# Kernel optimization log

Hardware: AMD Instinct MI355X
Metric: run time of the kernel (lower is better)

## Reference

```python
import jax, jax.numpy as jnp
import numpy as np

B, C_IN, H, W = 128, 2, 64, 64
K = 50  # value-iteration steps


def _conv(x, w, b=None):
    # NCHW input, OIHW weights, stride 1, SAME padding (odd kernel)
    y = jax.lax.conv_general_dilated(
        x, w, window_strides=(1, 1), padding='SAME',
        dimension_numbers=('NCHW', 'OIHW', 'NCHW'))
    if b is not None:
        y = y + b[None, :, None, None]
    return y


def setup_inputs() -> dict:
    key = jax.random.key(0)
    ks = jax.random.split(key, 10)
    pos_x = jax.random.randint(ks[0], (B,), 0, H, dtype=jnp.int32)
    pos_y = jax.random.randint(ks[1], (B,), 0, W, dtype=jnp.int32)
    # channel 0 encodes agent position (single >0 entry); channel 1 is the obstacle/goal map
    ch0 = jnp.zeros((B, H, W), jnp.float32).at[jnp.arange(B), pos_x, pos_y].set(1.0)
    ch1 = jax.random.normal(ks[2], (B, H, W), jnp.float32)
    x = jnp.stack([ch0, ch1], axis=1)  # [B, 2, H, W]
    sc = lambda *s: 1.0 / np.sqrt(np.prod(s[1:])) if len(s) > 1 else 0.1
    h_w = jax.random.normal(ks[3], (150, C_IN, 3, 3), jnp.float32) * sc(150, C_IN, 3, 3)
    h_b = jax.random.normal(ks[4], (150,), jnp.float32) * 0.1
    r_w = jax.random.normal(ks[5], (1, 150, 3, 3), jnp.float32) * sc(1, 150, 3, 3)
    r_b = jax.random.normal(ks[6], (1,), jnp.float32) * 0.1
    q_w = jax.random.normal(ks[7], (10, 2, 3, 3), jnp.float32) * sc(10, 2, 3, 3)
    q_b = jax.random.normal(ks[8], (10,), jnp.float32) * 0.1
    fc_w = jax.random.normal(ks[9], (8, 10), jnp.float32) * sc(8, 10)
    return {'x': x, 'pos_x': pos_x, 'pos_y': pos_y,
            'h_w': h_w, 'h_b': h_b, 'r_w': r_w, 'r_b': r_b,
            'q_w': q_w, 'q_b': q_b, 'fc_w': fc_w}


def reference(x, pos_x, pos_y, h_w, h_b, r_w, r_b, q_w, q_b, fc_w):
    h = _conv(x, h_w, h_b)            # [B, 150, H, W]
    r = _conv(h, r_w, r_b)            # [B, 1, H, W]
    v0 = jnp.zeros_like(r)

    def vi_step(v, _):
        q = _conv(jnp.concatenate([r, v], axis=1), q_w, q_b)  # [B, 10, H, W]
        return jnp.max(q, axis=1, keepdims=True), None

    v, _ = jax.lax.scan(vi_step, v0, None, length=K)
    q = _conv(jnp.concatenate([r, v], axis=1), q_w, q_b)      # [B, 10, H, W]
    q_at = q[jnp.arange(q.shape[0]), :, pos_x, pos_y]         # [B, 10]
    return q_at @ fc_w.T                                       # [B, 8]
```

## Files before the change

kernel.cpp:

```cpp
#include <hip/hip_runtime.h>

#define KI 50

#define X1_OFF 4624
#define R_OFF 9248
#define W_OFF 13736
#define LDS_TOT 14178

__device__ __forceinline__ void vi_step(const float* __restrict__ cur, float* __restrict__ nxt,
                                        int row, int c0,
                                        const float (&qr)[10][8], const float (&qwv)[10][9]) {
    float nb[3][12];
#pragma unroll
    for (int dy = 0; dy < 3; ++dy) {
        const float* lp = cur + (row + dy) * 68 + c0;
        float4 a0 = *(const float4*)lp;
        float4 a1 = *(const float4*)(lp + 4);
        float4 a2 = *(const float4*)(lp + 8);
        nb[dy][0] = a0.x; nb[dy][1] = a0.y; nb[dy][2]  = a0.z; nb[dy][3]  = a0.w;
        nb[dy][4] = a1.x; nb[dy][5] = a1.y; nb[dy][6]  = a1.z; nb[dy][7]  = a1.w;
        nb[dy][8] = a2.x; nb[dy][9] = a2.y; nb[dy][10] = a2.z; nb[dy][11] = a2.w;
    }
    float vmax[8];
#pragma unroll
    for (int c = 0; c < 10; ++c) {
#pragma unroll
        for (int p = 0; p < 8; ++p) {
            float acc = qr[c][p];
#pragma unroll
            for (int ky = 0; ky < 3; ++ky)
#pragma unroll
                for (int kx = 0; kx < 3; ++kx)
                    acc = fmaf(qwv[c][ky * 3 + kx], nb[ky][p + kx + 1], acc);
            vmax[p] = c ? fmaxf(vmax[p], acc) : acc;
        }
    }
    float* wp = nxt + (row + 1) * 68 + 2 + c0;
#pragma unroll
    for (int j = 0; j < 4; ++j)
        *(float2*)(wp + 2 * j) = make_float2(vmax[2 * j], vmax[2 * j + 1]);
}

__launch_bounds__(512, 2)
__global__ void vin_main(const float* __restrict__ x,
                         const int* __restrict__ pos_x, const int* __restrict__ pos_y,
                         const float* __restrict__ h_w, const float* __restrict__ h_b,
                         const float* __restrict__ r_w, const float* __restrict__ r_b,
                         const float* __restrict__ q_w, const float* __restrict__ q_b,
                         const float* __restrict__ fc_w, float* __restrict__ out) {
    __shared__ __align__(16) float S[LDS_TOT];
    const int tid = threadIdx.x;
    const int b = blockIdx.x;
    const int row = tid >> 3;
    const int c0 = (tid & 7) << 3;
    float* SW = S + W_OFF;

    float4 z4 = make_float4(0.f, 0.f, 0.f, 0.f);
    for (int i = tid; i < 3434; i += 512) ((float4*)S)[i] = z4;
    __syncthreads();

    {
        const float4* xg = (const float4*)(x + (size_t)b * 8192);
        for (int i = tid; i < 2048; i += 512) {
            float4 v = xg[i];
            int ch = i >> 10, rem = i & 1023;
            int y = rem >> 4, xc = (rem & 15) << 2;
            float* dst = S + ch * 4624 + (y + 2) * 68 + xc + 2;
            *(float2*)dst       = make_float2(v.x, v.y);
            *(float2*)(dst + 2) = make_float2(v.z, v.w);
        }
    }
    if (tid < 162) {
        int i = tid / 81, rem = tid % 81, dq = rem / 9, ds = rem % 9;
        float s = 0.f;
        for (int m = 0; m < 150; ++m)
            s = fmaf(r_w[m * 9 + dq], h_w[(m * 2 + i) * 9 + ds], s);
        SW[tid] = s;
    } else if (tid < 171) {
        int dq = tid - 162;
        float s = 0.f;
        for (int m = 0; m < 150; ++m)
            s = fmaf(r_w[m * 9 + dq], h_b[m], s);
        SW[tid] = s;
    } else if (tid < 351) {
        SW[tid] = q_w[tid - 171];
    } else if (tid < 361) {
        SW[tid] = q_b[tid - 351];
    } else if (tid < 441) {
        SW[tid] = fc_w[tid - 361];
    } else if (tid == 441) {
        SW[441] = r_b[0];
    }
    __syncthreads();

    {
        float xb0[5][12], xb1[5][12];
        const float* X0 = S;
        const float* X1 = S + X1_OFF;
#pragma unroll
        for (int dy = 0; dy < 5; ++dy) {
#pragma unroll
            for (int j = 0; j < 3; ++j) {
                float4 a = *(const float4*)&X0[(row + dy) * 68 + c0 + 4 * j];
                xb0[dy][4 * j + 0] = a.x; xb0[dy][4 * j + 1] = a.y;
                xb0[dy][4 * j + 2] = a.z; xb0[dy][4 * j + 3] = a.w;
                float4 c = *(const float4*)&X1[(row + dy) * 68 + c0 + 4 * j];
                xb1[dy][4 * j + 0] = c.x; xb1[dy][4 * j + 1] = c.y;
                xb1[dy][4 * j + 2] = c.z; xb1[dy][4 * j + 3] = c.w;
            }
        }
        float racc[8];
        float rbv = SW[441];
#pragma unroll
        for (int p = 0; p < 8; ++p) racc[p] = rbv;
#pragma unroll
        for (int dqy = 0; dqy < 3; ++dqy) {
            bool rowok = (row + dqy >= 1) && (row + dqy <= 64);
#pragma unroll
            for (int dqx = 0; dqx < 3; ++dqx) {
                int dq = dqy * 3 + dqx;
                float rh = SW[162 + dq];
                float w20[9], w21[9];
#pragma unroll
                for (int ds = 0; ds < 9; ++ds) {
                    w20[ds] = SW[dq * 9 + ds];
                    w21[ds] = SW[81 + dq * 9 + ds];
                }
#pragma unroll
                for (int p = 0; p < 8; ++p) {
                    float t = rh;
#pragma unroll
                    for (int dsy = 0; dsy < 3; ++dsy)
#pragma unroll
                        for (int dsx = 0; dsx < 3; ++dsx) {
                            int ds = dsy * 3 + dsx;
                            t = fmaf(w20[ds], xb0[dqy + dsy][p + dqx + dsx], t);
                            t = fmaf(w21[ds], xb1[dqy + dsy][p + dqx + dsx], t);
                        }
                    int qx = c0 + p + dqx - 1;
                    bool ok = rowok && (qx >= 0) && (qx < 64);
                    racc[p] += ok ? t : 0.f;
                }
            }
        }
#pragma unroll
        for (int p = 0; p < 8; ++p)
            S[R_OFF + (row + 1) * 68 + 2 + c0 + p] = racc[p];
    }
    __syncthreads();

    float qr[10][8];
    float qwv[10][9];
    {
        float rnb[3][12];
        const float* SR = S + R_OFF;
#pragma unroll
        for (int ky = 0; ky < 3; ++ky) {
            const float* lp = SR + (row + ky) * 68 + c0;
            float4 a0 = *(const float4*)lp;
            float4 a1 = *(const float4*)(lp + 4);
            float4 a2 = *(const float4*)(lp + 8);
            rnb[ky][0] = a0.x; rnb[ky][1] = a0.y; rnb[ky][2]  = a0.z; rnb[ky][3]  = a0.w;
            rnb[ky][4] = a1.x; rnb[ky][5] = a1.y; rnb[ky][6]  = a1.z; rnb[ky][7]  = a1.w;
            rnb[ky][8] = a2.x; rnb[ky][9] = a2.y; rnb[ky][10] = a2.z; rnb[ky][11] = a2.w;
        }
#pragma unroll
        for (int c = 0; c < 10; ++c) {
            float qbc = SW[351 + c];
            float w[9];
#pragma unroll
            for (int j = 0; j < 9; ++j) w[j] = SW[171 + c * 18 + j];
#pragma unroll
            for (int p = 0; p < 8; ++p) {
                float acc = qbc;
#pragma unroll
                for (int ky = 0; ky < 3; ++ky)
#pragma unroll
                    for (int kx = 0; kx < 3; ++kx)
                        acc = fmaf(w[ky * 3 + kx], rnb[ky][p + kx + 1], acc);
                qr[c][p] = acc;
            }
        }
#pragma unroll
        for (int c = 0; c < 10; ++c)
#pragma unroll
            for (int j = 0; j < 9; ++j) qwv[c][j] = SW[171 + c * 18 + 9 + j];
        for (int i = tid; i < 2312; i += 512) ((float4*)S)[i] = z4;
    }
    __syncthreads();

    float* vA = S;
    float* vB = S + X1_OFF;
#pragma unroll 1
    for (int k = 0; k < KI / 2; ++k) {
        vi_step(vA, vB, row, c0, qr, qwv);
        __syncthreads();
        vi_step(vB, vA, row, c0, qr, qwv);
        __syncthreads();
    }

    int pr = pos_x[b], pc = pos_y[b];
    if (row == pr && (pc >> 3) == (tid & 7)) {
        int p = pc & 7;
        float qf[10];
#pragma unroll
        for (int c = 0; c < 10; ++c) {
            float acc = qr[c][p];
#pragma unroll
            for (int ky = 0; ky < 3; ++ky)
#pragma unroll
                for (int kx = 0; kx < 3; ++kx)
                    acc = fmaf(qwv[c][3 * ky + kx], vA[(pr + ky) * 68 + pc + 1 + kx], acc);
            qf[c] = acc;
        }
#pragma unroll
        for (int o = 0; o < 8; ++o) {
            float s = 0.f;
#pragma unroll
            for (int c = 0; c < 10; ++c) s = fmaf(SW[361 + o * 10 + c], qf[c], s);
            out[b * 8 + o] = s;
        }
    }
}

extern "C" void kernel_launch(void* const* d_in, const int* in_sizes, int n_in,
                              void* d_out, int out_size, void* d_ws, size_t ws_size,
                              hipStream_t stream) {
    const float* x     = (const float*)d_in[0];
    const int*   pos_x = (const int*)d_in[1];
    const int*   pos_y = (const int*)d_in[2];
    const float* h_w   = (const float*)d_in[3];
    const float* h_b   = (const float*)d_in[4];
    const float* r_w   = (const float*)d_in[5];
    const float* r_b   = (const float*)d_in[6];
    const float* q_w   = (const float*)d_in[7];
    const float* q_b   = (const float*)d_in[8];
    const float* fc_w  = (const float*)d_in[9];
    float* out = (float*)d_out;

    vin_main<<<128, 512, 0, stream>>>(x, pos_x, pos_y, h_w, h_b, r_w, r_b,
                                      q_w, q_b, fc_w, out);
}
```

Measured before the change: 219.7 us.

## Read VI weights from LDS per step, stage weight folding through LDS

The value-iteration loop now loads its v-channel conv weights from LDS as float4s (padded to 12 per channel) instead of keeping 90 weights in registers. This frees VGPRs, and the launch bound is relaxed to one block per SIMD group. The r_w/h_w/h_b folding now reads from LDS copies instead of strided global loads. Zeroing of the R plane is cut down to its halo only, and one barrier is removed. The cost is extra LDS traffic on every VI step, in exchange for lower register pressure and less setup time.

```diff
diff --git a/kernel.cpp b/kernel.cpp
--- a/kernel.cpp
+++ b/kernel.cpp
@@ -5,11 +5,11 @@
 #define X1_OFF 4624
 #define R_OFF 9248
 #define W_OFF 13736
-#define LDS_TOT 14178
+#define LDS_TOT 14208
 
 __device__ __forceinline__ void vi_step(const float* __restrict__ cur, float* __restrict__ nxt,
-                                        int row, int c0,
-                                        const float (&qr)[10][8], const float (&qwv)[10][9]) {
+                                        const float* __restrict__ SW,
+                                        int row, int c0, const float (&qr)[10][8]) {
     float nb[3][12];
 #pragma unroll
     for (int dy = 0; dy < 3; ++dy) {
@@ -24,6 +24,9 @@
     float vmax[8];
 #pragma unroll
     for (int c = 0; c < 10; ++c) {
+        const float4* wc = (const float4*)(SW + 352 + c * 12);
+        float4 w0 = wc[0], w1 = wc[1], w2v = wc[2];
+        float w[9] = {w0.x, w0.y, w0.z, w0.w, w1.x, w1.y, w1.z, w1.w, w2v.x};
 #pragma unroll
         for (int p = 0; p < 8; ++p) {
             float acc = qr[c][p];
@@ -31,7 +34,7 @@
             for (int ky = 0; ky < 3; ++ky)
 #pragma unroll
                 for (int kx = 0; kx < 3; ++kx)
-                    acc = fmaf(qwv[c][ky * 3 + kx], nb[ky][p + kx + 1], acc);
+                    acc = fmaf(w[ky * 3 + kx], nb[ky][p + kx + 1], acc);
             vmax[p] = c ? fmaxf(vmax[p], acc) : acc;
         }
     }
@@ -41,7 +44,7 @@
         *(float2*)(wp + 2 * j) = make_float2(vmax[2 * j], vmax[2 * j + 1]);
 }
 
-__launch_bounds__(512, 2)
+__launch_bounds__(512, 1)
 __global__ void vin_main(const float* __restrict__ x,
                          const int* __restrict__ pos_x, const int* __restrict__ pos_y,
                          const float* __restrict__ h_w, const float* __restrict__ h_b,
@@ -54,10 +57,10 @@
     const int row = tid >> 3;
     const int c0 = (tid & 7) << 3;
     float* SW = S + W_OFF;
+    float* RL = S + R_OFF;
 
     float4 z4 = make_float4(0.f, 0.f, 0.f, 0.f);
-    for (int i = tid; i < 3434; i += 512) ((float4*)S)[i] = z4;
-    __syncthreads();
+    for (int i = tid; i < 2312; i += 512) ((float4*)S)[i] = z4;
 
     {
         const float4* xg = (const float4*)(x + (size_t)b * 8192);
@@ -69,30 +72,48 @@
             *(float2*)dst       = make_float2(v.x, v.y);
             *(float2*)(dst + 2) = make_float2(v.z, v.w);
         }
-    }
+        for (int i = tid; i < 1350; i += 512) RL[i] = r_w[i];
+        for (int i = tid; i < 2700; i += 512) RL[1350 + i] = h_w[i];
+        if (tid < 150) RL[4050 + tid] = h_b[tid];
+    }
+    __syncthreads();
+
     if (tid < 162) {
         int i = tid / 81, rem = tid % 81, dq = rem / 9, ds = rem % 9;
         float s = 0.f;
+#pragma unroll 5
         for (int m = 0; m < 150; ++m)
-            s = fmaf(r_w[m * 9 + dq], h_w[(m * 2 + i) * 9 + ds], s);
+            s = fmaf(RL[m * 9 + dq], RL[1350 + (m * 2 + i) * 9 + ds], s);
         SW[tid] = s;
     } else if (tid < 171) {
         int dq = tid - 162;
         float s = 0.f;
+#pragma unroll 5
         for (int m = 0; m < 150; ++m)
-            s = fmaf(r_w[m * 9 + dq], h_b[m], s);
+            s = fmaf(RL[m * 9 + dq], RL[4050 + m], s);
         SW[tid] = s;
-    } else if (tid < 351) {
-        SW[tid] = q_w[tid - 171];
-    } else if (tid < 361) {
-        SW[tid] = q_b[tid - 351];
-    } else if (tid < 441) {
-        SW[tid] = fc_w[tid - 361];
-    } else if (tid == 441) {
-        SW[441] = r_b[0];
-    }
-    __syncthreads();
-
+    } else if (tid < 181) {
+        SW[tid] = q_b[tid - 171];
+    } else if (tid == 181) {
+        SW[181] = r_b[0];
+    } else if (tid < 262) {
+        SW[tid] = fc_w[tid - 182];
+    } else if (tid < 352) {
+        int t = tid - 262;
+        SW[tid] = q_w[(t / 9) * 18 + (t % 9)];
+    } else if (tid < 472) {
+        int t = tid - 352, c = t / 12, j = t % 12;
+        SW[tid] = (j < 9) ? q_w[c * 18 + 9 + j] : 0.f;
+    }
+    __syncthreads();
+
+    if (tid < 34) {
+        int rrow = (tid < 17) ? 0 : 65;
+        *(float4*)&S[R_OFF + rrow * 68 + (tid % 17) * 4] = z4;
+    } else if (tid >= 64 && tid < 192) {
+        int t = tid - 64, r = 1 + (t & 63), side = t >> 6;
+        *(float2*)&S[R_OFF + r * 68 + (side ? 66 : 0)] = make_float2(0.f, 0.f);
+    }
     {
         float xb0[5][12], xb1[5][12];
         const float* X0 = S;
@@ -110,7 +131,7 @@
             }
         }
         float racc[8];
-        float rbv = SW[441];
+        float rbv = SW[181];
 #pragma unroll
         for (int p = 0; p < 8; ++p) racc[p] = rbv;
 #pragma unroll
@@ -143,14 +164,14 @@
                 }
             }
         }
-#pragma unroll
-        for (int p = 0; p < 8; ++p)
-            S[R_OFF + (row + 1) * 68 + 2 + c0 + p] = racc[p];
+        float* wp = S + R_OFF + (row + 1) * 68 + 2 + c0;
+#pragma unroll
+        for (int j = 0; j < 4; ++j)
+            *(float2*)(wp + 2 * j) = make_float2(racc[2 * j], racc[2 * j + 1]);
     }
     __syncthreads();
 
     float qr[10][8];
-    float qwv[10][9];
     {
         float rnb[3][12];
         const float* SR = S + R_OFF;
@@ -166,10 +187,10 @@
         }
 #pragma unroll
         for (int c = 0; c < 10; ++c) {
-            float qbc = SW[351 + c];
+            float qbc = SW[171 + c];
             float w[9];
 #pragma unroll
-            for (int j = 0; j < 9; ++j) w[j] = SW[171 + c * 18 + j];
+            for (int j = 0; j < 9; ++j) w[j] = SW[262 + c * 9 + j];
 #pragma unroll
             for (int p = 0; p < 8; ++p) {
                 float acc = qbc;
@@ -181,10 +202,6 @@
                 qr[c][p] = acc;
             }
         }
-#pragma unroll
-        for (int c = 0; c < 10; ++c)
-#pragma unroll
-            for (int j = 0; j < 9; ++j) qwv[c][j] = SW[171 + c * 18 + 9 + j];
         for (int i = tid; i < 2312; i += 512) ((float4*)S)[i] = z4;
     }
     __syncthreads();
@@ -193,9 +210,9 @@
     float* vB = S + X1_OFF;
 #pragma unroll 1
     for (int k = 0; k < KI / 2; ++k) {
-        vi_step(vA, vB, row, c0, qr, qwv);
+        vi_step(vA, vB, SW, row, c0, qr);
         __syncthreads();
-        vi_step(vB, vA, row, c0, qr, qwv);
+        vi_step(vB, vA, SW, row, c0, qr);
         __syncthreads();
     }
 
@@ -210,14 +227,15 @@
             for (int ky = 0; ky < 3; ++ky)
 #pragma unroll
                 for (int kx = 0; kx < 3; ++kx)
-                    acc = fmaf(qwv[c][3 * ky + kx], vA[(pr + ky) * 68 + pc + 1 + kx], acc);
+                    acc = fmaf(SW[352 + c * 12 + 3 * ky + kx],
+                               vA[(pr + ky) * 68 + pc + 1 + kx], acc);
             qf[c] = acc;
         }
 #pragma unroll
         for (int o = 0; o < 8; ++o) {
             float s = 0.f;
 #pragma unroll
-            for (int c = 0; c < 10; ++c) s = fmaf(SW[361 + o * 10 + c], qf[c], s);
+            for (int c = 0; c < 10; ++c) s = fmaf(SW[182 + o * 10 + c], qf[c], s);
             out[b * 8 + o] = s;
         }
     }
```

Result: slower. 230.7 us (+5.0%).
